# Optimization experiments

Hardware: AMD Instinct MI355X
Metric: run time of the kernel (lower is better)

Reference implementation:

```python
import jax, jax.numpy as jnp
import numpy as np

N = 100000   # nodes
E = 1250000  # edges
IN = 64
HID = 64
OUT = 64


def setup_inputs() -> dict:
    key = jax.random.key(0)
    ks = jax.random.split(key, 8)
    x = jax.random.normal(ks[0], (N, IN), dtype=jnp.float32)
    edge_index = jax.random.randint(ks[1], (2, E), 0, N, dtype=jnp.int64)
    s_in = 1.0 / np.sqrt(IN)
    s_h = 1.0 / np.sqrt(HID)
    W1 = jax.random.normal(ks[2], (IN, HID), dtype=jnp.float32) * s_in
    b1 = jnp.zeros((HID,), dtype=jnp.float32)
    W2 = jax.random.normal(ks[3], (HID, HID), dtype=jnp.float32) * s_h
    b2 = jnp.zeros((HID,), dtype=jnp.float32)
    Wp = jax.random.normal(ks[4], (HID, OUT), dtype=jnp.float32) * s_h
    bp = jnp.zeros((OUT,), dtype=jnp.float32)
    return {"x": x, "edge_index": edge_index, "W1": W1, "b1": b1,
            "W2": W2, "b2": b2, "Wp": Wp, "bp": bp}


def _gcn_conv(h, W, b, src, dst, inv_sqrt_deg):
    # PyG GCNConv with add_self_loops: x' = D^{-1/2} (A+I) D^{-1/2} (h W) + b
    m = h @ W                                   # [N, F]
    norm = inv_sqrt_deg[src] * inv_sqrt_deg[dst]  # [E]
    agg = jax.ops.segment_sum(m[src] * norm[:, None], dst, num_segments=N)
    agg = agg + m * (inv_sqrt_deg * inv_sqrt_deg)[:, None]  # self-loop term (norm = 1/deg)
    return agg + b


def reference(x, edge_index, W1, b1, W2, b2, Wp, bp):
    src = edge_index[0]
    dst = edge_index[1]
    # degree with self-loops (edge weight 1)
    deg = jax.ops.segment_sum(jnp.ones((E,), dtype=x.dtype), dst, num_segments=N) + 1.0
    inv_sqrt_deg = jax.lax.rsqrt(deg)
    # dropout is identity in eval mode
    h = jax.nn.relu(_gcn_conv(x, W1, b1, src, dst, inv_sqrt_deg))
    h = jax.nn.relu(_gcn_conv(h, W2, b2, src, dst, inv_sqrt_deg))
    z = h @ Wp + bp                             # [N, OUT]
    return z
```

## Files before the change

kernel.cpp:

```cpp
#include <hip/hip_runtime.h>

#define F 64
#define NPART 256
#define CAP 8192

typedef unsigned short u16x8 __attribute__((ext_vector_type(8)));
typedef _Float16       f16x8 __attribute__((ext_vector_type(8)));
typedef float          f32x4 __attribute__((ext_vector_type(4)));

__device__ __forceinline__ float h2f(unsigned short u) {
    _Float16 h; __builtin_memcpy(&h, &u, 2); return (float)h;
}
__device__ __forceinline__ unsigned short f2h(float f) {
    _Float16 h = (_Float16)f; unsigned short u; __builtin_memcpy(&u, &h, 2); return u;
}


__global__ void k_binit(int* bbase) {
    bbase[threadIdx.x * 16] = threadIdx.x * CAP;
}

template<int EPT>
__global__ __launch_bounds__(256)
void k_bin(const int* __restrict__ src, const int* __restrict__ dst,
           int* bbase, int2* staging, int nE, int nN) {
    __shared__ int lcnt[NPART];
    __shared__ int lbase[NPART];
    const int t  = threadIdx.x;
    const int i0 = blockIdx.x * 256 * EPT;
    lcnt[t] = 0;
    __syncthreads();
    int es[EPT], ed[EPT], bk[EPT];
#pragma unroll
    for (int k = 0; k < EPT; ++k) {
        const int i = i0 + k * 256 + t;
        if (i < nE) {
            es[k] = src[i];
            ed[k] = dst[i];
            bk[k] = (int)(((long long)ed[k] * NPART) / nN);
            atomicAdd(&lcnt[bk[k]], 1);
        } else bk[k] = -1;
    }
    __syncthreads();
    lbase[t] = atomicAdd(&bbase[t * 16], lcnt[t]);
    lcnt[t] = 0;
    __syncthreads();
#pragma unroll
    for (int k = 0; k < EPT; ++k) {
        if (bk[k] >= 0) {
            const int r   = atomicAdd(&lcnt[bk[k]], 1);
            const int pos = lbase[bk[k]] + r;
            if (pos < (bk[k] + 1) * CAP)
                staging[pos] = make_int2(es[k], ed[k]);
        }
    }
}

__global__ __launch_bounds__(256)
void k_sortP(const int2* __restrict__ staging, const int* __restrict__ bbase,
             int* __restrict__ ebs, int* __restrict__ rowptr,
             float* __restrict__ isd, int nN, int nE) {
    __shared__ int pc[NPART];
    __shared__ int pcv[NPART];
    __shared__ int cnt[512];
    __shared__ int cur[512];
    const int p = blockIdx.x;
    const int t = threadIdx.x;

    int cval = bbase[t * 16] - t * CAP;
    if (cval > CAP) cval = CAP;
    if (cval < 0)   cval = 0;
    pc[t]  = cval;
    pcv[t] = cval;
    __syncthreads();
#pragma unroll
    for (int off = 1; off < NPART; off <<= 1) {
        const int a = (t >= off) ? pc[t - off] : 0;
        __syncthreads();
        pc[t] += a;
        __syncthreads();
    }
    const int cg    = pcv[p];
    const int ebase = pc[p] - cg;
    const int lo    = (int)(((long long)nN * p + NPART - 1) / NPART);
    const int hi    = (int)(((long long)nN * (p + 1) + NPART - 1) / NPART);
    const int npn   = hi - lo;

    cnt[t] = 0; cnt[t + 256] = 0;
    __syncthreads();
    const int2* st = staging + (size_t)p * CAP;
    for (int j = t; j < cg; j += 256) atomicAdd(&cnt[st[j].y - lo], 1);
    __syncthreads();

    const int c0 = cnt[t], c1 = cnt[t + 256];
#pragma unroll
    for (int off = 1; off < 512; off <<= 1) {
        const int a0 = (t >= off) ? cnt[t - off] : 0;
        const int a1 = (t + 256 >= off) ? cnt[t + 256 - off] : 0;
        __syncthreads();
        cnt[t] += a0; cnt[t + 256] += a1;
        __syncthreads();
    }
    const int e0 = cnt[t] - c0, e1 = cnt[t + 256] - c1;
    cur[t] = e0; cur[t + 256] = e1;

    if (t < npn)        { rowptr[lo + t]        = ebase + e0; isd[lo + t]        = rsqrtf((float)c0 + 1.0f); }
    if (t + 256 < npn)  { rowptr[lo + t + 256]  = ebase + e1; isd[lo + t + 256]  = rsqrtf((float)c1 + 1.0f); }
    if (p == NPART - 1 && t == 0) rowptr[nN] = ebase + cg;
    __syncthreads();

    for (int j = t; j < cg; j += 256) {
        const int2 e = st[j];
        const int  r = atomicAdd(&cur[e.y - lo], 1);
        ebs[ebase + r] = e.x;
    }
}


__global__ __launch_bounds__(256)
void k_agg(const unsigned short* __restrict__ mh, const float* __restrict__ isd,
           const int* __restrict__ rowptr, const int* __restrict__ ebs,
           unsigned short* __restrict__ aggh, int nN) {
    const int n = (blockIdx.x * 256 + threadIdx.x) >> 6;
    const int l = threadIdx.x & 63;
    if (n >= nN) return;
    const int beg = __builtin_amdgcn_readfirstlane(rowptr[n]);
    const int end = __builtin_amdgcn_readfirstlane(rowptr[n + 1]);
    const float di = isd[n];
    const float self = h2f(mh[(size_t)n * F + l]) * di * di;
    float a0 = 0.f, a1 = 0.f, a2 = 0.f, a3 = 0.f;
    int e = beg;
    for (; e + 8 <= end; e += 8) {
        const int s0 = ebs[e + 0], s1 = ebs[e + 1], s2 = ebs[e + 2], s3 = ebs[e + 3];
        const int s4 = ebs[e + 4], s5 = ebs[e + 5], s6 = ebs[e + 6], s7 = ebs[e + 7];
        const float w0 = isd[s0], w1 = isd[s1], w2 = isd[s2], w3 = isd[s3];
        const float w4 = isd[s4], w5 = isd[s5], w6 = isd[s6], w7 = isd[s7];
        const float v0 = h2f(mh[(size_t)s0 * F + l]);
        const float v1 = h2f(mh[(size_t)s1 * F + l]);
        const float v2 = h2f(mh[(size_t)s2 * F + l]);
        const float v3 = h2f(mh[(size_t)s3 * F + l]);
        const float v4 = h2f(mh[(size_t)s4 * F + l]);
        const float v5 = h2f(mh[(size_t)s5 * F + l]);
        const float v6 = h2f(mh[(size_t)s6 * F + l]);
        const float v7 = h2f(mh[(size_t)s7 * F + l]);
        a0 = fmaf(v0, w0, a0);
        a1 = fmaf(v1, w1, a1);
        a2 = fmaf(v2, w2, a2);
        a3 = fmaf(v3, w3, a3);
        a0 = fmaf(v4, w4, a0);
        a1 = fmaf(v5, w5, a1);
        a2 = fmaf(v6, w6, a2);
        a3 = fmaf(v7, w7, a3);
    }
    for (; e + 2 <= end; e += 2) {
        const int s0 = ebs[e + 0], s1 = ebs[e + 1];
        a0 = fmaf(h2f(mh[(size_t)s0 * F + l]), isd[s0], a0);
        a1 = fmaf(h2f(mh[(size_t)s1 * F + l]), isd[s1], a1);
    }
    if (e < end) {
        const int s0 = ebs[e];
        a2 = fmaf(h2f(mh[(size_t)s0 * F + l]), isd[s0], a2);
    }
    aggh[(size_t)n * F + l] = f2h(fmaf((a0 + a1) + (a2 + a3), di, self));
}


template<bool RBIN, bool BOUT, bool INH, bool OUTH>
__global__ __launch_bounds__(256)
void k_gemm(const float* inf, const unsigned short* inh,
            const float* __restrict__ W,
            const float* __restrict__ bin, const float* __restrict__ bout,
            float* outf, unsigned short* outh, int nTiles)
{
    __shared__ _Float16 Wt[64 * 72];
    const int t = threadIdx.x;
#pragma unroll
    for (int i = 0; i < 16; ++i) {
        const int idx = i * 256 + t;
        const int k = idx >> 6, c = idx & 63;
        Wt[c * 72 + k] = (_Float16)W[idx];
    }
    __syncthreads();

    const int w    = t >> 6;
    const int l    = t & 63;
    const int lr   = l & 15;
    const int lg   = l >> 4;
    const int tile = blockIdx.x * 4 + w;
    if (tile >= nTiles) return;

    f16x8 bf[2][4];
#pragma unroll
    for (int kt = 0; kt < 2; ++kt)
#pragma unroll
        for (int ct = 0; ct < 4; ++ct)
            bf[kt][ct] = *(const f16x8*)&Wt[(ct * 16 + lr) * 72 + kt * 32 + lg * 8];

    f16x8 af[2];
    const int n = tile * 16 + lr;
    if (INH) {
        const unsigned short* rp = inh + (size_t)n * F;
#pragma unroll
        for (int kt = 0; kt < 2; ++kt) {
            u16x8 v = *(const u16x8*)(rp + kt * 32 + lg * 8);
            if (RBIN) {
                const int k0 = kt * 32 + lg * 8;
                const float4 blv = *(const float4*)(bin + k0);
                const float4 bhv = *(const float4*)(bin + k0 + 4);
                const float bb[8] = {blv.x, blv.y, blv.z, blv.w, bhv.x, bhv.y, bhv.z, bhv.w};
                f16x8 a;
#pragma unroll
                for (int j = 0; j < 8; ++j)
                    a[j] = (_Float16)fmaxf(h2f(v[j]) + bb[j], 0.f);
                af[kt] = a;
            } else {
                af[kt] = *(f16x8*)&v;
            }
        }
    } else {
        const float* rp = inf + (size_t)n * F;
#pragma unroll
        for (int kt = 0; kt < 2; ++kt) {
            const float4 v0 = *(const float4*)(rp + kt * 32 + lg * 8);
            const float4 v1 = *(const float4*)(rp + kt * 32 + lg * 8 + 4);
            f16x8 a;
            a[0] = (_Float16)v0.x; a[1] = (_Float16)v0.y;
            a[2] = (_Float16)v0.z; a[3] = (_Float16)v0.w;
            a[4] = (_Float16)v1.x; a[5] = (_Float16)v1.y;
            a[6] = (_Float16)v1.z; a[7] = (_Float16)v1.w;
            af[kt] = a;
        }
    }

    f32x4 acc[4] = {{0.f,0.f,0.f,0.f},{0.f,0.f,0.f,0.f},{0.f,0.f,0.f,0.f},{0.f,0.f,0.f,0.f}};
#pragma unroll
    for (int kt = 0; kt < 2; ++kt)
#pragma unroll
        for (int ct = 0; ct < 4; ++ct)
            acc[ct] = __builtin_amdgcn_mfma_f32_16x16x32_f16(af[kt], bf[kt][ct], acc[ct], 0, 0, 0);

    const int rowb = tile * 16 + lg * 4;
#pragma unroll
    for (int ct = 0; ct < 4; ++ct) {
        const int c = ct * 16 + lr;
        float badd = 0.f;
        if (BOUT) badd = bout[c];
#pragma unroll
        for (int r = 0; r < 4; ++r) {
            const float v = acc[ct][r] + badd;
            if (OUTH) outh[(size_t)(rowb + r) * F + c] = f2h(v);
            else      outf[(size_t)(rowb + r) * F + c] = v;
        }
    }
}


extern "C" void kernel_launch(void* const* d_in, const int* in_sizes, int n_in,
                              void* d_out, int out_size, void* d_ws, size_t ws_size,
                              hipStream_t stream)
{
    const float* x   = (const float*)d_in[0];
    const int*   ei  = (const int*)d_in[1];
    const float* W1  = (const float*)d_in[2];
    const float* b1  = (const float*)d_in[3];
    const float* W2  = (const float*)d_in[4];
    const float* b2  = (const float*)d_in[5];
    const float* Wp  = (const float*)d_in[6];
    const float* bp  = (const float*)d_in[7];
    float*       z   = (float*)d_out;

    const int nN = in_sizes[0] / F;
    const int nE = in_sizes[1] / 2;
    const int* srcp = ei;
    const int* dstp = ei + nE;

    char* ws = (char*)d_ws;
    size_t o = 0;
    auto alloc = [&](size_t bytes) { char* p = ws + o; o += (bytes + 255) & ~(size_t)255; return p; };
    float* isd    = (float*)alloc((size_t)nN * 4);
    int*   rowptr = (int*)  alloc(((size_t)nN + 1) * 4);
    int*   bbase  = (int*)  alloc((size_t)NPART * 16 * 4);
    int*   ebs    = (int*)  alloc((size_t)nE * 4);
    char*  U      = alloc((size_t)nN * F * 2 * 2 > (size_t)NPART * CAP * 8
                          ? (size_t)nN * F * 2 * 2 : (size_t)NPART * CAP * 8);
    int2*  staging = (int2*)U;
    unsigned short* mh   = (unsigned short*)U;
    unsigned short* aggh = (unsigned short*)(U + (size_t)nN * F * 2);

    const int gbA = (nN * 64 + 255) / 256;
    constexpr int EPT = 16;
    const int gbB = (nE + 256 * EPT - 1) / (256 * EPT);
    const int nTiles = nN / 16;
    const int gbG = (nTiles + 3) / 4;

    k_binit<<<1, NPART, 0, stream>>>(bbase);
    k_bin<EPT><<<gbB, 256, 0, stream>>>(srcp, dstp, bbase, staging, nE, nN);
    k_sortP<<<NPART, 256, 0, stream>>>(staging, bbase, ebs, rowptr, isd, nN, nE);

    k_gemm<false, false, false, true><<<gbG, 256, 0, stream>>>(x, nullptr, W1, nullptr, nullptr, nullptr, mh, nTiles);
    k_agg<<<gbA, 256, 0, stream>>>(mh, isd, rowptr, ebs, aggh, nN);

    k_gemm<true, false, true, true><<<gbG, 256, 0, stream>>>(nullptr, aggh, W2, b1, nullptr, nullptr, mh, nTiles);
    k_agg<<<gbA, 256, 0, stream>>>(mh, isd, rowptr, ebs, aggh, nN);

    k_gemm<true, true, true, false><<<gbG, 256, 0, stream>>>(nullptr, aggh, Wp, b2, bp, z, nullptr, nTiles);
}
```

Baseline: 156.0 us.

## Fuse aggregation with following GEMM and co-launch binning with first GEMM

The first GEMM now shares one launch with the edge-binning kernel: the extra blocks do x·W1 while the others bin edges. Each sparse aggregation is fused with the GEMM that follows it. A block aggregates 64 nodes, applies bias and ReLU, stores the fp16 rows in LDS, then runs the MFMA on them. This drops the aggh intermediate's round trip through global memory and cuts the launch count from 8 to 5. The cost is that each wave now walks 16 nodes one after another and the grid is much smaller, so fewer gathers may be in flight to hide latency.

```diff
diff --git a/kernel.cpp b/kernel.cpp
--- a/kernel.cpp
+++ b/kernel.cpp
@@ -22,36 +22,94 @@
 
 template<int EPT>
 __global__ __launch_bounds__(256)
-void k_bin(const int* __restrict__ src, const int* __restrict__ dst,
-           int* bbase, int2* staging, int nE, int nN) {
+void k_binGemm1(const int* __restrict__ src, const int* __restrict__ dst,
+                int* bbase, int2* staging,
+                const float* __restrict__ x, const float* __restrict__ W1,
+                unsigned short* __restrict__ mhA,
+                int nE, int nN, int nBin, int nTiles)
+{
     __shared__ int lcnt[NPART];
     __shared__ int lbase[NPART];
-    const int t  = threadIdx.x;
-    const int i0 = blockIdx.x * 256 * EPT;
-    lcnt[t] = 0;
-    __syncthreads();
-    int es[EPT], ed[EPT], bk[EPT];
-#pragma unroll
-    for (int k = 0; k < EPT; ++k) {
-        const int i = i0 + k * 256 + t;
-        if (i < nE) {
-            es[k] = src[i];
-            ed[k] = dst[i];
-            bk[k] = (int)(((long long)ed[k] * NPART) / nN);
-            atomicAdd(&lcnt[bk[k]], 1);
-        } else bk[k] = -1;
-    }
-    __syncthreads();
-    lbase[t] = atomicAdd(&bbase[t * 16], lcnt[t]);
-    lcnt[t] = 0;
-    __syncthreads();
-#pragma unroll
-    for (int k = 0; k < EPT; ++k) {
-        if (bk[k] >= 0) {
-            const int r   = atomicAdd(&lcnt[bk[k]], 1);
-            const int pos = lbase[bk[k]] + r;
-            if (pos < (bk[k] + 1) * CAP)
-                staging[pos] = make_int2(es[k], ed[k]);
+    __shared__ _Float16 Wt[64 * 72];
+    const int t = threadIdx.x;
+
+    if (blockIdx.x < nBin) {
+        const int i0 = blockIdx.x * 256 * EPT;
+        lcnt[t] = 0;
+        __syncthreads();
+        int es[EPT], ed[EPT], bk[EPT];
+#pragma unroll
+        for (int k = 0; k < EPT; ++k) {
+            const int i = i0 + k * 256 + t;
+            if (i < nE) {
+                es[k] = src[i];
+                ed[k] = dst[i];
+                bk[k] = (int)(((long long)ed[k] * NPART) / nN);
+                atomicAdd(&lcnt[bk[k]], 1);
+            } else bk[k] = -1;
+        }
+        __syncthreads();
+        lbase[t] = atomicAdd(&bbase[t * 16], lcnt[t]);
+        lcnt[t] = 0;
+        __syncthreads();
+#pragma unroll
+        for (int k = 0; k < EPT; ++k) {
+            if (bk[k] >= 0) {
+                const int r   = atomicAdd(&lcnt[bk[k]], 1);
+                const int pos = lbase[bk[k]] + r;
+                if (pos < (bk[k] + 1) * CAP)
+                    staging[pos] = make_int2(es[k], ed[k]);
+            }
+        }
+    } else {
+#pragma unroll
+        for (int i = 0; i < 16; ++i) {
+            const int idx = i * 256 + t;
+            Wt[(idx & 63) * 72 + (idx >> 6)] = (_Float16)W1[idx];
+        }
+        __syncthreads();
+        const int w    = t >> 6;
+        const int l    = t & 63;
+        const int lr   = l & 15;
+        const int lg   = l >> 4;
+        const int tile = (blockIdx.x - nBin) * 4 + w;
+        if (tile >= nTiles) return;
+
+        f16x8 bf[2][4];
+#pragma unroll
+        for (int kt = 0; kt < 2; ++kt)
+#pragma unroll
+            for (int ct = 0; ct < 4; ++ct)
+                bf[kt][ct] = *(const f16x8*)&Wt[(ct * 16 + lr) * 72 + kt * 32 + lg * 8];
+
+        const float* rp = x + (size_t)(tile * 16 + lr) * F;
+        f16x8 af[2];
+#pragma unroll
+        for (int kt = 0; kt < 2; ++kt) {
+            const float4 v0 = *(const float4*)(rp + kt * 32 + lg * 8);
+            const float4 v1 = *(const float4*)(rp + kt * 32 + lg * 8 + 4);
+            f16x8 a;
+            a[0] = (_Float16)v0.x; a[1] = (_Float16)v0.y;
+            a[2] = (_Float16)v0.z; a[3] = (_Float16)v0.w;
+            a[4] = (_Float16)v1.x; a[5] = (_Float16)v1.y;
+            a[6] = (_Float16)v1.z; a[7] = (_Float16)v1.w;
+            af[kt] = a;
+        }
+
+        f32x4 acc[4] = {{0.f,0.f,0.f,0.f},{0.f,0.f,0.f,0.f},{0.f,0.f,0.f,0.f},{0.f,0.f,0.f,0.f}};
+#pragma unroll
+        for (int kt = 0; kt < 2; ++kt)
+#pragma unroll
+            for (int ct = 0; ct < 4; ++ct)
+                acc[ct] = __builtin_amdgcn_mfma_f32_16x16x32_f16(af[kt], bf[kt][ct], acc[ct], 0, 0, 0);
+
+        const int rowb = tile * 16 + lg * 4;
+#pragma unroll
+        for (int ct = 0; ct < 4; ++ct) {
+            const int c = ct * 16 + lr;
+#pragma unroll
+            for (int r = 0; r < 4; ++r)
+                mhA[(size_t)(rowb + r) * F + c] = f2h(acc[ct][r]);
         }
     }
 }
@@ -117,77 +175,80 @@
 }
 
 
+template<bool PROJ>
 __global__ __launch_bounds__(256)
-void k_agg(const unsigned short* __restrict__ mh, const float* __restrict__ isd,
-           const int* __restrict__ rowptr, const int* __restrict__ ebs,
-           unsigned short* __restrict__ aggh, int nN) {
-    const int n = (blockIdx.x * 256 + threadIdx.x) >> 6;
-    const int l = threadIdx.x & 63;
-    if (n >= nN) return;
-    const int beg = __builtin_amdgcn_readfirstlane(rowptr[n]);
-    const int end = __builtin_amdgcn_readfirstlane(rowptr[n + 1]);
-    const float di = isd[n];
-    const float self = h2f(mh[(size_t)n * F + l]) * di * di;
-    float a0 = 0.f, a1 = 0.f, a2 = 0.f, a3 = 0.f;
-    int e = beg;
-    for (; e + 8 <= end; e += 8) {
-        const int s0 = ebs[e + 0], s1 = ebs[e + 1], s2 = ebs[e + 2], s3 = ebs[e + 3];
-        const int s4 = ebs[e + 4], s5 = ebs[e + 5], s6 = ebs[e + 6], s7 = ebs[e + 7];
-        const float w0 = isd[s0], w1 = isd[s1], w2 = isd[s2], w3 = isd[s3];
-        const float w4 = isd[s4], w5 = isd[s5], w6 = isd[s6], w7 = isd[s7];
-        const float v0 = h2f(mh[(size_t)s0 * F + l]);
-        const float v1 = h2f(mh[(size_t)s1 * F + l]);
-        const float v2 = h2f(mh[(size_t)s2 * F + l]);
-        const float v3 = h2f(mh[(size_t)s3 * F + l]);
-        const float v4 = h2f(mh[(size_t)s4 * F + l]);
-        const float v5 = h2f(mh[(size_t)s5 * F + l]);
-        const float v6 = h2f(mh[(size_t)s6 * F + l]);
-        const float v7 = h2f(mh[(size_t)s7 * F + l]);
-        a0 = fmaf(v0, w0, a0);
-        a1 = fmaf(v1, w1, a1);
-        a2 = fmaf(v2, w2, a2);
-        a3 = fmaf(v3, w3, a3);
-        a0 = fmaf(v4, w4, a0);
-        a1 = fmaf(v5, w5, a1);
-        a2 = fmaf(v6, w6, a2);
-        a3 = fmaf(v7, w7, a3);
-    }
-    for (; e + 2 <= end; e += 2) {
-        const int s0 = ebs[e + 0], s1 = ebs[e + 1];
-        a0 = fmaf(h2f(mh[(size_t)s0 * F + l]), isd[s0], a0);
-        a1 = fmaf(h2f(mh[(size_t)s1 * F + l]), isd[s1], a1);
-    }
-    if (e < end) {
-        const int s0 = ebs[e];
-        a2 = fmaf(h2f(mh[(size_t)s0 * F + l]), isd[s0], a2);
-    }
-    aggh[(size_t)n * F + l] = f2h(fmaf((a0 + a1) + (a2 + a3), di, self));
-}
-
-
-template<bool RBIN, bool BOUT, bool INH, bool OUTH>
-__global__ __launch_bounds__(256)
-void k_gemm(const float* inf, const unsigned short* inh,
-            const float* __restrict__ W,
-            const float* __restrict__ bin, const float* __restrict__ bout,
-            float* outf, unsigned short* outh, int nTiles)
+void k_aggGemm(const unsigned short* __restrict__ mhIn,
+               const float* __restrict__ isd,
+               const int* __restrict__ rowptr, const int* __restrict__ ebs,
+               const float* __restrict__ W, const float* __restrict__ bin,
+               const float* __restrict__ bout,
+               unsigned short* __restrict__ outh, float* __restrict__ outf,
+               int nN)
 {
     __shared__ _Float16 Wt[64 * 72];
+    __shared__ _Float16 A[64 * 72];
     const int t = threadIdx.x;
 #pragma unroll
     for (int i = 0; i < 16; ++i) {
         const int idx = i * 256 + t;
-        const int k = idx >> 6, c = idx & 63;
-        Wt[c * 72 + k] = (_Float16)W[idx];
-    }
-    __syncthreads();
-
-    const int w    = t >> 6;
-    const int l    = t & 63;
-    const int lr   = l & 15;
-    const int lg   = l >> 4;
-    const int tile = blockIdx.x * 4 + w;
-    if (tile >= nTiles) return;
+        Wt[(idx & 63) * 72 + (idx >> 6)] = (_Float16)W[idx];
+    }
+
+    const int w  = t >> 6;
+    const int l  = t & 63;
+    const int nb = blockIdx.x * 64;
+    const float bl = bin[l];
+
+    for (int i = 0; i < 16; ++i) {
+        const int n = nb + w * 16 + i;
+        if (n < nN) {
+            const int beg = __builtin_amdgcn_readfirstlane(rowptr[n]);
+            const int end = __builtin_amdgcn_readfirstlane(rowptr[n + 1]);
+            const float di = isd[n];
+            const float self = h2f(mhIn[(size_t)n * F + l]) * di * di;
+            float a0 = 0.f, a1 = 0.f, a2 = 0.f, a3 = 0.f;
+            int e = beg;
+            for (; e + 8 <= end; e += 8) {
+                const int s0 = ebs[e + 0], s1 = ebs[e + 1], s2 = ebs[e + 2], s3 = ebs[e + 3];
+                const int s4 = ebs[e + 4], s5 = ebs[e + 5], s6 = ebs[e + 6], s7 = ebs[e + 7];
+                const float w0 = isd[s0], w1 = isd[s1], w2 = isd[s2], w3 = isd[s3];
+                const float w4 = isd[s4], w5 = isd[s5], w6 = isd[s6], w7 = isd[s7];
+                const float v0 = h2f(mhIn[(size_t)s0 * F + l]);
+                const float v1 = h2f(mhIn[(size_t)s1 * F + l]);
+                const float v2 = h2f(mhIn[(size_t)s2 * F + l]);
+                const float v3 = h2f(mhIn[(size_t)s3 * F + l]);
+                const float v4 = h2f(mhIn[(size_t)s4 * F + l]);
+                const float v5 = h2f(mhIn[(size_t)s5 * F + l]);
+                const float v6 = h2f(mhIn[(size_t)s6 * F + l]);
+                const float v7 = h2f(mhIn[(size_t)s7 * F + l]);
+                a0 = fmaf(v0, w0, a0);
+                a1 = fmaf(v1, w1, a1);
+                a2 = fmaf(v2, w2, a2);
+                a3 = fmaf(v3, w3, a3);
+                a0 = fmaf(v4, w4, a0);
+                a1 = fmaf(v5, w5, a1);
+                a2 = fmaf(v6, w6, a2);
+                a3 = fmaf(v7, w7, a3);
+            }
+            for (; e + 2 <= end; e += 2) {
+                const int s0 = ebs[e + 0], s1 = ebs[e + 1];
+                a0 = fmaf(h2f(mhIn[(size_t)s0 * F + l]), isd[s0], a0);
+                a1 = fmaf(h2f(mhIn[(size_t)s1 * F + l]), isd[s1], a1);
+            }
+            if (e < end) {
+                const int s0 = ebs[e];
+                a2 = fmaf(h2f(mhIn[(size_t)s0 * F + l]), isd[s0], a2);
+            }
+            const float v = fmaf((a0 + a1) + (a2 + a3), di, self);
+            A[(w * 16 + i) * 72 + l] = (_Float16)fmaxf(v + bl, 0.f);
+        }
+    }
+    __syncthreads();
+
+    const int rowt = nb + w * 16;
+    if (rowt >= nN) return;
+    const int lr = l & 15;
+    const int lg = l >> 4;
 
     f16x8 bf[2][4];
 #pragma unroll
@@ -197,40 +258,9 @@
             bf[kt][ct] = *(const f16x8*)&Wt[(ct * 16 + lr) * 72 + kt * 32 + lg * 8];
 
     f16x8 af[2];
-    const int n = tile * 16 + lr;
-    if (INH) {
-        const unsigned short* rp = inh + (size_t)n * F;
-#pragma unroll
-        for (int kt = 0; kt < 2; ++kt) {
-            u16x8 v = *(const u16x8*)(rp + kt * 32 + lg * 8);
-            if (RBIN) {
-                const int k0 = kt * 32 + lg * 8;
-                const float4 blv = *(const float4*)(bin + k0);
-                const float4 bhv = *(const float4*)(bin + k0 + 4);
-                const float bb[8] = {blv.x, blv.y, blv.z, blv.w, bhv.x, bhv.y, bhv.z, bhv.w};
-                f16x8 a;
-#pragma unroll
-                for (int j = 0; j < 8; ++j)
-                    a[j] = (_Float16)fmaxf(h2f(v[j]) + bb[j], 0.f);
-                af[kt] = a;
-            } else {
-                af[kt] = *(f16x8*)&v;
-            }
-        }
-    } else {
-        const float* rp = inf + (size_t)n * F;
-#pragma unroll
-        for (int kt = 0; kt < 2; ++kt) {
-            const float4 v0 = *(const float4*)(rp + kt * 32 + lg * 8);
-            const float4 v1 = *(const float4*)(rp + kt * 32 + lg * 8 + 4);
-            f16x8 a;
-            a[0] = (_Float16)v0.x; a[1] = (_Float16)v0.y;
-            a[2] = (_Float16)v0.z; a[3] = (_Float16)v0.w;
-            a[4] = (_Float16)v1.x; a[5] = (_Float16)v1.y;
-            a[6] = (_Float16)v1.z; a[7] = (_Float16)v1.w;
-            af[kt] = a;
-        }
-    }
+#pragma unroll
+    for (int kt = 0; kt < 2; ++kt)
+        af[kt] = *(const f16x8*)&A[(w * 16 + lr) * 72 + kt * 32 + lg * 8];
 
     f32x4 acc[4] = {{0.f,0.f,0.f,0.f},{0.f,0.f,0.f,0.f},{0.f,0.f,0.f,0.f},{0.f,0.f,0.f,0.f}};
 #pragma unroll
@@ -239,17 +269,17 @@
         for (int ct = 0; ct < 4; ++ct)
             acc[ct] = __builtin_amdgcn_mfma_f32_16x16x32_f16(af[kt], bf[kt][ct], acc[ct], 0, 0, 0);
 
-    const int rowb = tile * 16 + lg * 4;
+    const int rowb = rowt + lg * 4;
 #pragma unroll
     for (int ct = 0; ct < 4; ++ct) {
         const int c = ct * 16 + lr;
         float badd = 0.f;
-        if (BOUT) badd = bout[c];
+        if (PROJ) badd = bout[c];
 #pragma unroll
         for (int r = 0; r < 4; ++r) {
             const float v = acc[ct][r] + badd;
-            if (OUTH) outh[(size_t)(rowb + r) * F + c] = f2h(v);
-            else      outf[(size_t)(rowb + r) * F + c] = v;
+            if (PROJ) outf[(size_t)(rowb + r) * F + c] = v;
+            else      outh[(size_t)(rowb + r) * F + c] = f2h(v);
         }
     }
 }
@@ -281,27 +311,24 @@
     int*   rowptr = (int*)  alloc(((size_t)nN + 1) * 4);
     int*   bbase  = (int*)  alloc((size_t)NPART * 16 * 4);
     int*   ebs    = (int*)  alloc((size_t)nE * 4);
-    char*  U      = alloc((size_t)nN * F * 2 * 2 > (size_t)NPART * CAP * 8
-                          ? (size_t)nN * F * 2 * 2 : (size_t)NPART * CAP * 8);
+    char*  U      = alloc((size_t)NPART * CAP * 8);
     int2*  staging = (int2*)U;
-    unsigned short* mh   = (unsigned short*)U;
-    unsigned short* aggh = (unsigned short*)(U + (size_t)nN * F * 2);
-
-    const int gbA = (nN * 64 + 255) / 256;
+    unsigned short* mhB = (unsigned short*)U;
+    unsigned short* mhA = (unsigned short*)alloc((size_t)nN * F * 2);
+
     constexpr int EPT = 16;
-    const int gbB = (nE + 256 * EPT - 1) / (256 * EPT);
+    const int gbB    = (nE + 256 * EPT - 1) / (256 * EPT);
     const int nTiles = nN / 16;
-    const int gbG = (nTiles + 3) / 4;
+    const int gbG    = (nTiles + 3) / 4;
+    const int gbF    = (nN + 63) / 64;
 
     k_binit<<<1, NPART, 0, stream>>>(bbase);
-    k_bin<EPT><<<gbB, 256, 0, stream>>>(srcp, dstp, bbase, staging, nE, nN);
+    k_binGemm1<EPT><<<gbB + gbG, 256, 0, stream>>>(srcp, dstp, bbase, staging,
+                                                   x, W1, mhA, nE, nN, gbB, nTiles);
     k_sortP<<<NPART, 256, 0, stream>>>(staging, bbase, ebs, rowptr, isd, nN, nE);
 
-    k_gemm<false, false, false, true><<<gbG, 256, 0, stream>>>(x, nullptr, W1, nullptr, nullptr, nullptr, mh, nTiles);
-    k_agg<<<gbA, 256, 0, stream>>>(mh, isd, rowptr, ebs, aggh, nN);
-
-    k_gemm<true, false, true, true><<<gbG, 256, 0, stream>>>(nullptr, aggh, W2, b1, nullptr, nullptr, mh, nTiles);
-    k_agg<<<gbA, 256, 0, stream>>>(mh, isd, rowptr, ebs, aggh, nN);
-
-    k_gemm<true, true, true, false><<<gbG, 256, 0, stream>>>(nullptr, aggh, Wp, b2, bp, z, nullptr, nTiles);
-}
+    k_aggGemm<false><<<gbF, 256, 0, stream>>>(mhA, isd, rowptr, ebs, W2, b1, nullptr,
+                                              mhB, nullptr, nN);
+    k_aggGemm<true><<<gbF, 256, 0, stream>>>(mhB, isd, rowptr, ebs, Wp, b2, bp,
+                                             nullptr, z, nN);
+}
```

Measured after the change: 145.5 us. 6.7% less time.
